# Performance work log

Measured on AMD Instinct MI355X. Metric: run time of the kernel, lower is better.

Reference implementation:

```python
import jax, jax.numpy as jnp
import numpy as np


def _wn(v, g):
    # weight norm over input axis: w[:, j] = g[j] * v[:, j] / ||v[:, j]||
    norm = jnp.sqrt(jnp.sum(v * v, axis=0, keepdims=True))
    return v * (g[None, :] / norm)


def setup_inputs() -> dict:
    key = jax.random.key(0)
    ks = jax.random.split(key, 6)
    M, K1, H, OUT = 65536, 512, 1024, 512
    x = jax.random.normal(ks[0], (M, K1), dtype=jnp.float32)
    v1 = jax.random.normal(ks[1], (K1, H), dtype=jnp.float32) * 0.05
    v2 = jax.random.normal(ks[2], (H, H), dtype=jnp.float32) * 0.05
    v3 = jax.random.normal(ks[3], (H, H), dtype=jnp.float32) * 0.05
    v4 = jax.random.normal(ks[4], (H, H), dtype=jnp.float32) * 0.05
    v5 = jax.random.normal(ks[5], (H, OUT), dtype=jnp.float32) * 0.05
    g1 = jnp.ones((H,), jnp.float32)
    g2 = jnp.ones((H,), jnp.float32)
    g3 = jnp.ones((H,), jnp.float32)
    g4 = jnp.ones((H,), jnp.float32)
    g5 = jnp.ones((OUT,), jnp.float32)
    return {"x": x, "v1": v1, "g1": g1, "v2": v2, "g2": g2,
            "v3": v3, "g3": g3, "v4": v4, "g4": g4, "v5": v5, "g5": g5}


def reference(x, v1, g1, v2, g2, v3, g3, v4, g4, v5, g5):
    w1 = _wn(v1, g1)
    w2 = _wn(v2, g2)
    w3 = _wn(v3, g3)
    w4 = _wn(v4, g4)
    w5 = _wn(v5, g5)
    h1 = jax.nn.softplus(x @ w1)    # [M, H]
    h2 = jax.nn.softplus(h1 @ w2)
    h3 = jax.nn.softplus(h2 @ w3)
    h4 = jax.nn.softplus(h3 @ w4)
    out = h4 @ w5                   # final layer linear
    return out
```

## Files before the change

kernel.cpp:

```cpp
#include <hip/hip_runtime.h>
#include <hip/hip_bf16.h>
#include <cstdint>

typedef unsigned short u16;
typedef __attribute__((ext_vector_type(8))) _Float16 f16x8;
typedef __attribute__((ext_vector_type(4))) float f32x4;
typedef __attribute__((ext_vector_type(8))) unsigned short u16x8;

typedef const __attribute__((address_space(1))) void* gas1p;
typedef __attribute__((address_space(3))) void* las3p;
typedef const __attribute__((address_space(3))) u16* lc16p;

__device__ __forceinline__ void gld_lds16(const void* g, void* l) {
    __builtin_amdgcn_global_load_lds((gas1p)g, (las3p)l, 16, 0, 0);
}

__device__ __forceinline__ f16x8 dsr128(const u16* p) {
    f16x8 r;
    asm volatile("ds_read_b128 %0, %1" : "=v"(r) : "v"((lc16p)p));
    return r;
}

__device__ __forceinline__ u16 f2h(float f) {
    _Float16 h = (_Float16)f;
    return __builtin_bit_cast(u16, h);
}

__global__ void cvt_x_kernel(const float4* __restrict__ x, u16* __restrict__ xb) {
    size_t i = (size_t)blockIdx.x * blockDim.x + threadIdx.x;
    float4 a = x[2 * i];
    float4 b = x[2 * i + 1];
    u16x8 o;
    o[0] = f2h(a.x); o[1] = f2h(a.y); o[2] = f2h(a.z); o[3] = f2h(a.w);
    o[4] = f2h(b.x); o[5] = f2h(b.y); o[6] = f2h(b.z); o[7] = f2h(b.w);
    *(u16x8*)&xb[i * 8] = o;
}

struct WnDesc {
    const float* v; const float* g; u16* wT; float* partial;
    int K; int N; int blk0;
};
struct WnPack { WnDesc d[5]; int nlayer; };

__global__ void wn_partial_all(WnPack p) {
    int b = blockIdx.x;
    int l = 0;
    while (l + 1 < p.nlayer && b >= p.d[l + 1].blk0) l++;
    const WnDesc& d = p.d[l];
    int lb = b - d.blk0;
    int nbx = d.N >> 6;
    int bx = lb % nbx, seg = lb / nbx;

    int lane = threadIdx.x & 63;
    int tr = threadIdx.x >> 6;
    int n = bx * 64 + lane;
    int kseg = d.K >> 3;
    int kbeg = seg * kseg;
    float s = 0.f;
    for (int k = kbeg + tr; k < kbeg + kseg; k += 4) {
        float x = d.v[(size_t)k * d.N + n];
        s += x * x;
    }
    __shared__ float red[4][64];
    red[tr][lane] = s;
    __syncthreads();
    if (tr == 0)
        d.partial[seg * d.N + n] = red[0][lane] + red[1][lane] + red[2][lane] + red[3][lane];
}

__global__ void wn_write_all(WnPack p) {
    int b = blockIdx.x;
    int l = 0;
    while (l + 1 < p.nlayer && b >= p.d[l + 1].blk0) l++;
    const WnDesc& d = p.d[l];
    int lb = b - d.blk0;
    int nbx = d.N >> 6;
    int bx = lb % nbx, seg = lb / nbx;

    int lane = threadIdx.x & 63;
    int tr = threadIdx.x >> 6;
    int n = bx * 64 + lane;
    float s = 0.f;
#pragma unroll
    for (int i = 0; i < 8; i++) s += d.partial[i * d.N + n];
    float sc = d.g[n] / sqrtf(s);

    int kseg = d.K >> 3;
    int kbeg = seg * kseg;
    for (int k = kbeg + tr; k < kbeg + kseg; k += 4)
        d.wT[(size_t)n * d.K + k] = f2h(d.v[(size_t)k * d.N + n] * sc);
}

template<int N, int K, bool ACT, bool OUTF32>
__global__ __launch_bounds__(512, 2) void gemm_mlp(
    const u16* __restrict__ A, const u16* __restrict__ Bt,
    u16* __restrict__ Ch, float* __restrict__ Cf)
{
    constexpr int M = 65536;
    constexpr int NT = K / 64;
    constexpr int NTN = N / 256;
    constexpr int NWG = (M / 256) * NTN;

    __shared__ u16 sA[2][256 * 64];
    __shared__ u16 sB[2][2 * 128 * 64];

    const int bid = blockIdx.x;
    const int wk = (bid & 7) * (NWG >> 3) + (bid >> 3);
    const int tm = wk / NTN, tn = wk % NTN;
    const long m0 = (long)tm * 256;
    const int n0 = tn * 256;

    const int tid = threadIdx.x;
    const int lane = tid & 63;
    const int wid = tid >> 6;
    const int wm = (wid >> 2) * 128;
    const int wn = (wid & 3) * 64;

    const int r8 = tid >> 3;
    const int gcol = ((tid & 7) ^ (r8 & 7)) * 8;
    const u16* Abase = A + (m0 + r8) * (size_t)K + gcol;
    const u16* Bbase = Bt + (size_t)(n0 + ((r8 >> 5) * 64 + (r8 & 31))) * K + gcol;
    const int dst8 = tid * 8;

    auto stA0 = [&](int buf, int t) {
        gld_lds16(Abase + (size_t)t * 64, &sA[buf][0 * 4096 + dst8]);
        gld_lds16(Abase + (size_t)128 * K + (size_t)t * 64, &sA[buf][2 * 4096 + dst8]);
    };
    auto stA1 = [&](int buf, int t) {
        gld_lds16(Abase + (size_t)64 * K + (size_t)t * 64, &sA[buf][1 * 4096 + dst8]);
        gld_lds16(Abase + (size_t)192 * K + (size_t)t * 64, &sA[buf][3 * 4096 + dst8]);
    };
    auto stB0 = [&](int buf, int t) {
        gld_lds16(Bbase + (size_t)t * 64, &sB[buf][dst8]);
        gld_lds16(Bbase + (size_t)128 * K + (size_t)t * 64, &sB[buf][4096 + dst8]);
    };
    auto stB1 = [&](int buf, int t) {
        gld_lds16(Bbase + (size_t)32 * K + (size_t)t * 64, &sB[buf][8192 + dst8]);
        gld_lds16(Bbase + (size_t)160 * K + (size_t)t * 64, &sB[buf][8192 + 4096 + dst8]);
    };

    const int rbase = lane & 15;
    const int co0 = ((lane >> 4) ^ (lane & 7)) * 8;
    const int arow0 = (wm + rbase) * 64 + co0;
    const int brow0 = ((wn >> 6) * 32 + rbase) * 64 + co0;

    f32x4 acc[8][4] = {};
    f16x8 rA0[4][2], rA1[4][2], rB0[2][2], rB1[2][2];

    auto dsrA = [&](f16x8 (&r)[4][2], int buf, int qm) {
#pragma unroll
        for (int i = 0; i < 4; i++) {
            int base = arow0 + (qm * 64 + i * 16) * 64;
            r[i][0] = dsr128(&sA[buf][base]);
            r[i][1] = dsr128(&sA[buf][base ^ 32]);
        }
    };
    auto dsrB = [&](f16x8 (&r)[2][2], int buf, int qn) {
#pragma unroll
        for (int j2 = 0; j2 < 2; j2++) {
            int base = brow0 + qn * 8192 + j2 * 1024;
            r[j2][0] = dsr128(&sB[buf][base]);
            r[j2][1] = dsr128(&sB[buf][base ^ 32]);
        }
    };
    auto mm = [&](f16x8 (&ra)[4][2], f16x8 (&rb)[2][2], int qm, int qn) {
        __builtin_amdgcn_s_setprio(1);
#pragma unroll
        for (int kk = 0; kk < 2; kk++)
#pragma unroll
            for (int i = 0; i < 4; i++)
#pragma unroll
                for (int j2 = 0; j2 < 2; j2++)
                    acc[qm * 4 + i][qn * 2 + j2] = __builtin_amdgcn_mfma_f32_16x16x32_f16(
                        ra[i][kk], rb[j2][kk], acc[qm * 4 + i][qn * 2 + j2], 0, 0, 0);
        __builtin_amdgcn_s_setprio(0);
    };
    auto BAR = [&]() { __builtin_amdgcn_s_barrier(); };
#define LGKM(n) { asm volatile("s_waitcnt lgkmcnt(" #n ")"); __builtin_amdgcn_sched_barrier(0); }
#define VMCNT(n) { asm volatile("s_waitcnt vmcnt(" #n ")"); __builtin_amdgcn_sched_barrier(0); }

    stA0(0, 0); stB0(0, 0); stA1(0, 0); stB1(0, 0);
    stA0(1, 1); stB0(1, 1); stA1(1, 1); stB1(1, 1);
    VMCNT(8);
    BAR();
    dsrA(rA0, 0, 0); dsrB(rB0, 0, 0);
    LGKM(0);
    BAR();

    for (int t = 0; t < NT - 2; t++) {
        const int cur = t & 1, nxt = cur ^ 1;
        dsrB(rB1, cur, 1);
        stA0(cur, t + 2);
        BAR(); LGKM(4);
        mm(rA0, rB0, 0, 0);
        BAR();
        dsrA(rA1, cur, 1);
        stB0(cur, t + 2);
        BAR(); LGKM(8);
        mm(rA0, rB1, 0, 1);
        BAR();
        VMCNT(4);
        dsrA(rA0, nxt, 0);
        BAR(); LGKM(8);
        mm(rA1, rB0, 1, 0);
        BAR();
        dsrB(rB0, nxt, 0);
        stA1(cur, t + 2); stB1(cur, t + 2);
        BAR();
        mm(rA1, rB1, 1, 1);
        LGKM(4);
        BAR();
    }
    {
        const int cur = (NT - 2) & 1, nxt = cur ^ 1;
        dsrB(rB1, cur, 1);
        BAR(); LGKM(4);
        mm(rA0, rB0, 0, 0);
        BAR();
        dsrA(rA1, cur, 1);
        BAR(); LGKM(8);
        mm(rA0, rB1, 0, 1);
        BAR();
        VMCNT(0);
        dsrA(rA0, nxt, 0);
        BAR(); LGKM(8);
        mm(rA1, rB0, 1, 0);
        BAR();
        dsrB(rB0, nxt, 0);
        BAR();
        mm(rA1, rB1, 1, 1);
        LGKM(4);
        BAR();
    }
    {
        const int cur = (NT - 1) & 1;
        dsrB(rB1, cur, 1);
        BAR(); LGKM(4);
        mm(rA0, rB0, 0, 0);
        BAR();
        dsrA(rA1, cur, 1);
        BAR(); LGKM(8);
        mm(rA0, rB1, 0, 1);
        BAR();
        LGKM(0);
        mm(rA1, rB0, 1, 0);
        mm(rA1, rB1, 1, 1);
    }
#undef LGKM
#undef VMCNT

    const long crow0 = m0 + wm + ((lane >> 4) << 2);
    const int ccol0 = n0 + wn + (lane & 15);
#pragma unroll
    for (int fi = 0; fi < 8; fi++) {
#pragma unroll
        for (int r = 0; r < 4; r++) {
            const size_t rowoff = (size_t)(crow0 + fi * 16 + r) * N;
#pragma unroll
            for (int fj = 0; fj < 4; fj++) {
                float v = acc[fi][fj][r];
                if (ACT) v = fmaxf(v, 0.f) + __logf(1.f + __expf(-fabsf(v)));
                if (OUTF32) Cf[rowoff + ccol0 + fj * 16] = v;
                else        Ch[rowoff + ccol0 + fj * 16] = f2h(v);
            }
        }
    }
}

extern "C" void kernel_launch(void* const* d_in, const int* in_sizes, int n_in,
                              void* d_out, int out_size, void* d_ws, size_t ws_size,
                              hipStream_t stream) {
    const float* x  = (const float*)d_in[0];
    const float* v1 = (const float*)d_in[1];
    const float* g1 = (const float*)d_in[2];
    const float* v2 = (const float*)d_in[3];
    const float* g2 = (const float*)d_in[4];
    const float* v3 = (const float*)d_in[5];
    const float* g3 = (const float*)d_in[6];
    const float* v4 = (const float*)d_in[7];
    const float* g4 = (const float*)d_in[8];
    const float* v5 = (const float*)d_in[9];
    const float* g5 = (const float*)d_in[10];
    float* out = (float*)d_out;

    const int M = 65536;
    char* ws = (char*)d_ws;
    u16* bufA = (u16*)(ws);
    u16* bufB = (u16*)(ws + 0x8000000ULL);
    u16* w1T  = (u16*)(ws + 0x10000000ULL);
    u16* w2T  = w1T + 1024 * 512;
    u16* w3T  = w2T + 1024 * 1024;
    u16* w4T  = w3T + 1024 * 1024;
    u16* w5T  = w4T + 1024 * 1024;
    float* part = (float*)(ws + 0x10800000ULL);

    cvt_x_kernel<<<(M * 512) / (256 * 8), 256, 0, stream>>>((const float4*)x, bufB);

    WnPack pk;
    int cum = 0;
    auto mk = [&](int i, const float* v, const float* g, u16* wT, int K, int N) {
        pk.d[i] = WnDesc{v, g, wT, part + i * 8 * 1024, K, N, cum};
        cum += (N / 64) * 8;
    };
    mk(0, v1, g1, w1T, 512, 1024);
    mk(1, v2, g2, w2T, 1024, 1024);
    mk(2, v3, g3, w3T, 1024, 1024);
    mk(3, v4, g4, w4T, 1024, 1024);
    mk(4, v5, g5, w5T, 1024, 512);
    pk.nlayer = 5;

    wn_partial_all<<<cum, 256, 0, stream>>>(pk);
    wn_write_all<<<cum, 256, 0, stream>>>(pk);

    gemm_mlp<1024, 512,  true,  false><<<1024, 512, 0, stream>>>(bufB, w1T, bufA, nullptr);
    gemm_mlp<1024, 1024, true,  false><<<1024, 512, 0, stream>>>(bufA, w2T, bufB, nullptr);
    gemm_mlp<1024, 1024, true,  false><<<1024, 512, 0, stream>>>(bufB, w3T, bufA, nullptr);
    gemm_mlp<1024, 1024, true,  false><<<1024, 512, 0, stream>>>(bufA, w4T, bufB, nullptr);
    gemm_mlp<512,  1024, false, true ><<<512,  512, 0, stream>>>(bufB, w5T, nullptr, out);

    (void)in_sizes; (void)n_in; (void)out_size; (void)ws_size;
}
```

Measured before the change: 704.2 us.

## Make GEMMs walk all N tiles per row block with a continuous K pipeline

Each GEMM now launches 256 workgroups, one per 256-row block. Each workgroup loops over every 256-column N tile, and the double-buffered load/compute pipeline runs continuously across tile boundaries, with an in-loop epilogue that stores results and clears the accumulators. The goal is to remove pipeline prologue and drain costs at each tile and to keep the A row block hot in cache. The trade-off is that on a 256-CU part only one workgroup runs per CU, where the old launch had 1024 blocks at 2 per CU. The epilogue stores now also sit inside the pipeline, where they can stall the next tile's prefetch.

```diff
diff --git a/kernel.cpp b/kernel.cpp
--- a/kernel.cpp
+++ b/kernel.cpp
@@ -92,23 +92,23 @@
 }
 
 template<int N, int K, bool ACT, bool OUTF32>
-__global__ __launch_bounds__(512, 2) void gemm_mlp(
+__global__ __launch_bounds__(512, 2) void gemm_persist(
     const u16* __restrict__ A, const u16* __restrict__ Bt,
     u16* __restrict__ Ch, float* __restrict__ Cf)
 {
     constexpr int M = 65536;
-    constexpr int NT = K / 64;
+    constexpr int NTK = K / 64;
+    constexpr int LOGK = (NTK == 8) ? 3 : 4;
     constexpr int NTN = N / 256;
-    constexpr int NWG = (M / 256) * NTN;
+    constexpr int G = NTK * NTN;
+    constexpr int NWG = M / 256;
 
     __shared__ u16 sA[2][256 * 64];
     __shared__ u16 sB[2][2 * 128 * 64];
 
     const int bid = blockIdx.x;
     const int wk = (bid & 7) * (NWG >> 3) + (bid >> 3);
-    const int tm = wk / NTN, tn = wk % NTN;
-    const long m0 = (long)tm * 256;
-    const int n0 = tn * 256;
+    const long m0 = (long)wk * 256;
 
     const int tid = threadIdx.x;
     const int lane = tid & 63;
@@ -119,24 +119,28 @@
     const int r8 = tid >> 3;
     const int gcol = ((tid & 7) ^ (r8 & 7)) * 8;
     const u16* Abase = A + (m0 + r8) * (size_t)K + gcol;
-    const u16* Bbase = Bt + (size_t)(n0 + ((r8 >> 5) * 64 + (r8 & 31))) * K + gcol;
+    const u16* Bbase = Bt + (size_t)((r8 >> 5) * 64 + (r8 & 31)) * K + gcol;
     const int dst8 = tid * 8;
 
-    auto stA0 = [&](int buf, int t) {
-        gld_lds16(Abase + (size_t)t * 64, &sA[buf][0 * 4096 + dst8]);
-        gld_lds16(Abase + (size_t)128 * K + (size_t)t * 64, &sA[buf][2 * 4096 + dst8]);
-    };
-    auto stA1 = [&](int buf, int t) {
-        gld_lds16(Abase + (size_t)64 * K + (size_t)t * 64, &sA[buf][1 * 4096 + dst8]);
-        gld_lds16(Abase + (size_t)192 * K + (size_t)t * 64, &sA[buf][3 * 4096 + dst8]);
-    };
-    auto stB0 = [&](int buf, int t) {
-        gld_lds16(Bbase + (size_t)t * 64, &sB[buf][dst8]);
-        gld_lds16(Bbase + (size_t)128 * K + (size_t)t * 64, &sB[buf][4096 + dst8]);
-    };
-    auto stB1 = [&](int buf, int t) {
-        gld_lds16(Bbase + (size_t)32 * K + (size_t)t * 64, &sB[buf][8192 + dst8]);
-        gld_lds16(Bbase + (size_t)160 * K + (size_t)t * 64, &sB[buf][8192 + 4096 + dst8]);
+    auto aoff = [&](int gs) { return (size_t)(gs & (NTK - 1)) * 64; };
+    auto boff = [&](int gs) {
+        return (size_t)(gs >> LOGK) * ((size_t)256 * K) + (size_t)(gs & (NTK - 1)) * 64;
+    };
+    auto stA0 = [&](int buf, int gs) {
+        gld_lds16(Abase + aoff(gs), &sA[buf][dst8]);
+        gld_lds16(Abase + (size_t)128 * K + aoff(gs), &sA[buf][2 * 4096 + dst8]);
+    };
+    auto stA1 = [&](int buf, int gs) {
+        gld_lds16(Abase + (size_t)64 * K + aoff(gs), &sA[buf][1 * 4096 + dst8]);
+        gld_lds16(Abase + (size_t)192 * K + aoff(gs), &sA[buf][3 * 4096 + dst8]);
+    };
+    auto stB0 = [&](int buf, int gs) {
+        gld_lds16(Bbase + boff(gs), &sB[buf][dst8]);
+        gld_lds16(Bbase + (size_t)128 * K + boff(gs), &sB[buf][4096 + dst8]);
+    };
+    auto stB1 = [&](int buf, int gs) {
+        gld_lds16(Bbase + (size_t)32 * K + boff(gs), &sB[buf][8192 + dst8]);
+        gld_lds16(Bbase + (size_t)160 * K + boff(gs), &sB[buf][8192 + 4096 + dst8]);
     };
 
     const int rbase = lane & 15;
@@ -177,94 +181,81 @@
     };
     auto BAR = [&]() { __builtin_amdgcn_s_barrier(); };
 #define LGKM(n) { asm volatile("s_waitcnt lgkmcnt(" #n ")"); __builtin_amdgcn_sched_barrier(0); }
-#define VMCNT(n) { asm volatile("s_waitcnt vmcnt(" #n ")"); __builtin_amdgcn_sched_barrier(0); }
+#define VMC(n)  { asm volatile("s_waitcnt vmcnt(" #n ")");  __builtin_amdgcn_sched_barrier(0); }
+
+    auto epilogue = [&](int tn) {
+        const long crow0 = m0 + wm + ((lane >> 4) << 2);
+        const int ccol0 = tn * 256 + wn + (lane & 15);
+#pragma unroll
+        for (int fi = 0; fi < 8; fi++) {
+#pragma unroll
+            for (int r = 0; r < 4; r++) {
+                const size_t rowoff = (size_t)(crow0 + fi * 16 + r) * N;
+#pragma unroll
+                for (int fj = 0; fj < 4; fj++) {
+                    float v = acc[fi][fj][r];
+                    if (ACT) v = fmaxf(v, 0.f) + __logf(1.f + __expf(-fabsf(v)));
+                    if (OUTF32) Cf[rowoff + ccol0 + fj * 16] = v;
+                    else        Ch[rowoff + ccol0 + fj * 16] = f2h(v);
+                }
+            }
+        }
+#pragma unroll
+        for (int i = 0; i < 8; i++)
+#pragma unroll
+            for (int j = 0; j < 4; j++)
+                acc[i][j] = (f32x4){0.f, 0.f, 0.f, 0.f};
+    };
 
     stA0(0, 0); stB0(0, 0); stA1(0, 0); stB1(0, 0);
     stA0(1, 1); stB0(1, 1); stA1(1, 1); stB1(1, 1);
-    VMCNT(8);
+    VMC(4);
     BAR();
     dsrA(rA0, 0, 0); dsrB(rB0, 0, 0);
     LGKM(0);
     BAR();
 
-    for (int t = 0; t < NT - 2; t++) {
-        const int cur = t & 1, nxt = cur ^ 1;
+    for (int g = 0; g < G - 1; g++) {
+        const int cur = g & 1, nxt = cur ^ 1;
+        const bool st = (g < G - 2);
         dsrB(rB1, cur, 1);
-        stA0(cur, t + 2);
+        if (st) stA0(cur, g + 2);
         BAR(); LGKM(4);
         mm(rA0, rB0, 0, 0);
         BAR();
         dsrA(rA1, cur, 1);
-        stB0(cur, t + 2);
+        if (st) stB0(cur, g + 2);
         BAR(); LGKM(8);
         mm(rA0, rB1, 0, 1);
-        BAR();
-        VMCNT(4);
+        if (st) { VMC(4); } else { VMC(2); }
+        BAR();
         dsrA(rA0, nxt, 0);
         BAR(); LGKM(8);
         mm(rA1, rB0, 1, 0);
         BAR();
         dsrB(rB0, nxt, 0);
-        stA1(cur, t + 2); stB1(cur, t + 2);
+        if (st) { stA1(cur, g + 2); stB1(cur, g + 2); }
         BAR();
         mm(rA1, rB1, 1, 1);
-        LGKM(4);
-        BAR();
+        if (st) { VMC(4); } else { VMC(0); }
+        BAR();
+        if ((g & (NTK - 1)) == NTK - 1) epilogue(g >> LOGK);
     }
     {
-        const int cur = (NT - 2) & 1, nxt = cur ^ 1;
+        const int cur = (G - 1) & 1;
         dsrB(rB1, cur, 1);
-        BAR(); LGKM(4);
+        LGKM(4);
         mm(rA0, rB0, 0, 0);
-        BAR();
         dsrA(rA1, cur, 1);
-        BAR(); LGKM(8);
+        LGKM(8);
         mm(rA0, rB1, 0, 1);
-        BAR();
-        VMCNT(0);
-        dsrA(rA0, nxt, 0);
-        BAR(); LGKM(8);
-        mm(rA1, rB0, 1, 0);
-        BAR();
-        dsrB(rB0, nxt, 0);
-        BAR();
-        mm(rA1, rB1, 1, 1);
-        LGKM(4);
-        BAR();
-    }
-    {
-        const int cur = (NT - 1) & 1;
-        dsrB(rB1, cur, 1);
-        BAR(); LGKM(4);
-        mm(rA0, rB0, 0, 0);
-        BAR();
-        dsrA(rA1, cur, 1);
-        BAR(); LGKM(8);
-        mm(rA0, rB1, 0, 1);
-        BAR();
         LGKM(0);
         mm(rA1, rB0, 1, 0);
         mm(rA1, rB1, 1, 1);
+        epilogue(NTN - 1);
     }
 #undef LGKM
-#undef VMCNT
-
-    const long crow0 = m0 + wm + ((lane >> 4) << 2);
-    const int ccol0 = n0 + wn + (lane & 15);
-#pragma unroll
-    for (int fi = 0; fi < 8; fi++) {
-#pragma unroll
-        for (int r = 0; r < 4; r++) {
-            const size_t rowoff = (size_t)(crow0 + fi * 16 + r) * N;
-#pragma unroll
-            for (int fj = 0; fj < 4; fj++) {
-                float v = acc[fi][fj][r];
-                if (ACT) v = fmaxf(v, 0.f) + __logf(1.f + __expf(-fabsf(v)));
-                if (OUTF32) Cf[rowoff + ccol0 + fj * 16] = v;
-                else        Ch[rowoff + ccol0 + fj * 16] = f2h(v);
-            }
-        }
-    }
+#undef VMC
 }
 
 extern "C" void kernel_launch(void* const* d_in, const int* in_sizes, int n_in,
@@ -312,11 +303,11 @@
     wn_partial_all<<<cum, 256, 0, stream>>>(pk);
     wn_write_all<<<cum, 256, 0, stream>>>(pk);
 
-    gemm_mlp<1024, 512,  true,  false><<<1024, 512, 0, stream>>>(bufB, w1T, bufA, nullptr);
-    gemm_mlp<1024, 1024, true,  false><<<1024, 512, 0, stream>>>(bufA, w2T, bufB, nullptr);
-    gemm_mlp<1024, 1024, true,  false><<<1024, 512, 0, stream>>>(bufB, w3T, bufA, nullptr);
-    gemm_mlp<1024, 1024, true,  false><<<1024, 512, 0, stream>>>(bufA, w4T, bufB, nullptr);
-    gemm_mlp<512,  1024, false, true ><<<512,  512, 0, stream>>>(bufB, w5T, nullptr, out);
+    gemm_persist<1024, 512,  true,  false><<<256, 512, 0, stream>>>(bufB, w1T, bufA, nullptr);
+    gemm_persist<1024, 1024, true,  false><<<256, 512, 0, stream>>>(bufA, w2T, bufB, nullptr);
+    gemm_persist<1024, 1024, true,  false><<<256, 512, 0, stream>>>(bufB, w3T, bufA, nullptr);
+    gemm_persist<1024, 1024, true,  false><<<256, 512, 0, stream>>>(bufA, w4T, bufB, nullptr);
+    gemm_persist<512,  1024, false, true ><<<256, 512, 0, stream>>>(bufB, w5T, nullptr, out);
 
     (void)in_sizes; (void)n_in; (void)out_size; (void)ws_size;
 }
```

Measured after the change: 750.8 us. 1.07x slower.

## Load B fragments directly from global into registers, drop B LDS staging

Applied to the files above, without the earlier changes.

The GEMM no longer stages weight tiles in shared memory. Each wave now loads its B fragments straight from global memory into registers, while A stays double-buffered in LDS and is read with immediate-offset ds_read instructions. The pipeline becomes a simpler loop with one barrier per K step. This cuts LDS traffic and footprint, but each wave now issues redundant uncoalesced 16-byte global loads for B and has fewer in-flight stages to hide global latency.

```diff
diff --git a/kernel.cpp b/kernel.cpp
--- a/kernel.cpp
+++ b/kernel.cpp
@@ -15,9 +15,10 @@
     __builtin_amdgcn_global_load_lds((gas1p)g, (las3p)l, 16, 0, 0);
 }
 
-__device__ __forceinline__ f16x8 dsr128(const u16* p) {
+template<int OFF>
+__device__ __forceinline__ f16x8 dsr128o(const u16* p) {
     f16x8 r;
-    asm volatile("ds_read_b128 %0, %1" : "=v"(r) : "v"((lc16p)p));
+    asm volatile("ds_read_b128 %0, %1 offset:%2" : "=v"(r) : "v"((lc16p)p), "i"(OFF));
     return r;
 }
 
@@ -92,7 +93,7 @@
 }
 
 template<int N, int K, bool ACT, bool OUTF32>
-__global__ __launch_bounds__(512, 2) void gemm_mlp(
+__global__ __launch_bounds__(512, 2) void gemm_bl2(
     const u16* __restrict__ A, const u16* __restrict__ Bt,
     u16* __restrict__ Ch, float* __restrict__ Cf)
 {
@@ -102,7 +103,6 @@
     constexpr int NWG = (M / 256) * NTN;
 
     __shared__ u16 sA[2][256 * 64];
-    __shared__ u16 sB[2][2 * 128 * 64];
 
     const int bid = blockIdx.x;
     const int wk = (bid & 7) * (NWG >> 3) + (bid >> 3);
@@ -119,51 +119,33 @@
     const int r8 = tid >> 3;
     const int gcol = ((tid & 7) ^ (r8 & 7)) * 8;
     const u16* Abase = A + (m0 + r8) * (size_t)K + gcol;
-    const u16* Bbase = Bt + (size_t)(n0 + ((r8 >> 5) * 64 + (r8 & 31))) * K + gcol;
     const int dst8 = tid * 8;
-
-    auto stA0 = [&](int buf, int t) {
-        gld_lds16(Abase + (size_t)t * 64, &sA[buf][0 * 4096 + dst8]);
+    auto stA = [&](int buf, int t) {
+        gld_lds16(Abase + (size_t)t * 64, &sA[buf][dst8]);
         gld_lds16(Abase + (size_t)128 * K + (size_t)t * 64, &sA[buf][2 * 4096 + dst8]);
-    };
-    auto stA1 = [&](int buf, int t) {
         gld_lds16(Abase + (size_t)64 * K + (size_t)t * 64, &sA[buf][1 * 4096 + dst8]);
         gld_lds16(Abase + (size_t)192 * K + (size_t)t * 64, &sA[buf][3 * 4096 + dst8]);
-    };
-    auto stB0 = [&](int buf, int t) {
-        gld_lds16(Bbase + (size_t)t * 64, &sB[buf][dst8]);
-        gld_lds16(Bbase + (size_t)128 * K + (size_t)t * 64, &sB[buf][4096 + dst8]);
-    };
-    auto stB1 = [&](int buf, int t) {
-        gld_lds16(Bbase + (size_t)32 * K + (size_t)t * 64, &sB[buf][8192 + dst8]);
-        gld_lds16(Bbase + (size_t)160 * K + (size_t)t * 64, &sB[buf][8192 + 4096 + dst8]);
     };
 
     const int rbase = lane & 15;
     const int co0 = ((lane >> 4) ^ (lane & 7)) * 8;
     const int arow0 = (wm + rbase) * 64 + co0;
-    const int brow0 = ((wn >> 6) * 32 + rbase) * 64 + co0;
+
+    const int bn = n0 + wn + (lane & 15);
+    const int bk = (lane >> 4) * 8;
+    auto ldBg = [&](f16x8 (&dst)[2][2], int qn, int t) {
+#pragma unroll
+        for (int j2 = 0; j2 < 2; j2++)
+#pragma unroll
+            for (int kk = 0; kk < 2; kk++)
+                dst[j2][kk] = *(const f16x8*)&Bt[
+                    (size_t)(bn + qn * 32 + j2 * 16) * K + t * 64 + kk * 32 + bk];
+    };
 
     f32x4 acc[8][4] = {};
-    f16x8 rA0[4][2], rA1[4][2], rB0[2][2], rB1[2][2];
-
-    auto dsrA = [&](f16x8 (&r)[4][2], int buf, int qm) {
-#pragma unroll
-        for (int i = 0; i < 4; i++) {
-            int base = arow0 + (qm * 64 + i * 16) * 64;
-            r[i][0] = dsr128(&sA[buf][base]);
-            r[i][1] = dsr128(&sA[buf][base ^ 32]);
-        }
-    };
-    auto dsrB = [&](f16x8 (&r)[2][2], int buf, int qn) {
-#pragma unroll
-        for (int j2 = 0; j2 < 2; j2++) {
-            int base = brow0 + qn * 8192 + j2 * 1024;
-            r[j2][0] = dsr128(&sB[buf][base]);
-            r[j2][1] = dsr128(&sB[buf][base ^ 32]);
-        }
-    };
-    auto mm = [&](f16x8 (&ra)[4][2], f16x8 (&rb)[2][2], int qm, int qn) {
+    f16x8 rA0[4][2], rA1[4][2], B0[2][2], B1[2][2];
+
+    auto mmq = [&](f16x8 (&ra)[4][2], f16x8 (&rb)[2][2], int qm, int qn) {
         __builtin_amdgcn_s_setprio(1);
 #pragma unroll
         for (int kk = 0; kk < 2; kk++)
@@ -177,77 +159,51 @@
     };
     auto BAR = [&]() { __builtin_amdgcn_s_barrier(); };
 #define LGKM(n) { asm volatile("s_waitcnt lgkmcnt(" #n ")"); __builtin_amdgcn_sched_barrier(0); }
-#define VMCNT(n) { asm volatile("s_waitcnt vmcnt(" #n ")"); __builtin_amdgcn_sched_barrier(0); }
-
-    stA0(0, 0); stB0(0, 0); stA1(0, 0); stB1(0, 0);
-    stA0(1, 1); stB0(1, 1); stA1(1, 1); stB1(1, 1);
-    VMCNT(8);
+#define VMC(n)  { asm volatile("s_waitcnt vmcnt(" #n ")");  __builtin_amdgcn_sched_barrier(0); }
+
+    stA(0, 0);
+    ldBg(B0, 0, 0);
+    ldBg(B1, 1, 0);
+    VMC(8);
     BAR();
-    dsrA(rA0, 0, 0); dsrB(rB0, 0, 0);
-    LGKM(0);
-    BAR();
-
-    for (int t = 0; t < NT - 2; t++) {
+
+    for (int t = 0; t < NT; t++) {
         const int cur = t & 1, nxt = cur ^ 1;
-        dsrB(rB1, cur, 1);
-        stA0(cur, t + 2);
-        BAR(); LGKM(4);
-        mm(rA0, rB0, 0, 0);
-        BAR();
-        dsrA(rA1, cur, 1);
-        stB0(cur, t + 2);
-        BAR(); LGKM(8);
-        mm(rA0, rB1, 0, 1);
-        BAR();
-        VMCNT(4);
-        dsrA(rA0, nxt, 0);
-        BAR(); LGKM(8);
-        mm(rA1, rB0, 1, 0);
-        BAR();
-        dsrB(rB0, nxt, 0);
-        stA1(cur, t + 2); stB1(cur, t + 2);
-        BAR();
-        mm(rA1, rB1, 1, 1);
-        LGKM(4);
-        BAR();
-    }
-    {
-        const int cur = (NT - 2) & 1, nxt = cur ^ 1;
-        dsrB(rB1, cur, 1);
-        BAR(); LGKM(4);
-        mm(rA0, rB0, 0, 0);
-        BAR();
-        dsrA(rA1, cur, 1);
-        BAR(); LGKM(8);
-        mm(rA0, rB1, 0, 1);
-        BAR();
-        VMCNT(0);
-        dsrA(rA0, nxt, 0);
-        BAR(); LGKM(8);
-        mm(rA1, rB0, 1, 0);
-        BAR();
-        dsrB(rB0, nxt, 0);
-        BAR();
-        mm(rA1, rB1, 1, 1);
-        LGKM(4);
-        BAR();
-    }
-    {
-        const int cur = (NT - 1) & 1;
-        dsrB(rB1, cur, 1);
-        BAR(); LGKM(4);
-        mm(rA0, rB0, 0, 0);
-        BAR();
-        dsrA(rA1, cur, 1);
-        BAR(); LGKM(8);
-        mm(rA0, rB1, 0, 1);
-        BAR();
+        const bool more = (t + 1 < NT);
+
+        const u16* pA0 = &sA[cur][arow0];
+        const u16* pA1 = &sA[cur][arow0 ^ 32];
+#pragma unroll
+        for (int i = 0; i < 4; i++) {
+            if (i == 0) { rA0[0][0] = dsr128o<0>(pA0);     rA0[0][1] = dsr128o<0>(pA1); }
+            if (i == 1) { rA0[1][0] = dsr128o<2048>(pA0);  rA0[1][1] = dsr128o<2048>(pA1); }
+            if (i == 2) { rA0[2][0] = dsr128o<4096>(pA0);  rA0[2][1] = dsr128o<4096>(pA1); }
+            if (i == 3) { rA0[3][0] = dsr128o<6144>(pA0);  rA0[3][1] = dsr128o<6144>(pA1); }
+        }
+#pragma unroll
+        for (int i = 0; i < 4; i++) {
+            if (i == 0) { rA1[0][0] = dsr128o<8192>(pA0);  rA1[0][1] = dsr128o<8192>(pA1); }
+            if (i == 1) { rA1[1][0] = dsr128o<10240>(pA0); rA1[1][1] = dsr128o<10240>(pA1); }
+            if (i == 2) { rA1[2][0] = dsr128o<12288>(pA0); rA1[2][1] = dsr128o<12288>(pA1); }
+            if (i == 3) { rA1[3][0] = dsr128o<14336>(pA0); rA1[3][1] = dsr128o<14336>(pA1); }
+        }
+        if (more) stA(nxt, t + 1);
+
+        LGKM(8);
+        mmq(rA0, B0, 0, 0);
+        mmq(rA0, B1, 0, 1);
         LGKM(0);
-        mm(rA1, rB0, 1, 0);
-        mm(rA1, rB1, 1, 1);
+        mmq(rA1, B0, 1, 0);
+        if (more) ldBg(B0, 0, t + 1);
+        mmq(rA1, B1, 1, 1);
+        if (more) {
+            ldBg(B1, 1, t + 1);
+            VMC(8);
+            BAR();
+        }
     }
 #undef LGKM
-#undef VMCNT
+#undef VMC
 
     const long crow0 = m0 + wm + ((lane >> 4) << 2);
     const int ccol0 = n0 + wn + (lane & 15);
@@ -312,11 +268,11 @@
     wn_partial_all<<<cum, 256, 0, stream>>>(pk);
     wn_write_all<<<cum, 256, 0, stream>>>(pk);
 
-    gemm_mlp<1024, 512,  true,  false><<<1024, 512, 0, stream>>>(bufB, w1T, bufA, nullptr);
-    gemm_mlp<1024, 1024, true,  false><<<1024, 512, 0, stream>>>(bufA, w2T, bufB, nullptr);
-    gemm_mlp<1024, 1024, true,  false><<<1024, 512, 0, stream>>>(bufB, w3T, bufA, nullptr);
-    gemm_mlp<1024, 1024, true,  false><<<1024, 512, 0, stream>>>(bufA, w4T, bufB, nullptr);
-    gemm_mlp<512,  1024, false, true ><<<512,  512, 0, stream>>>(bufB, w5T, nullptr, out);
+    gemm_bl2<1024, 512,  true,  false><<<1024, 512, 0, stream>>>(bufB, w1T, bufA, nullptr);
+    gemm_bl2<1024, 1024, true,  false><<<1024, 512, 0, stream>>>(bufA, w2T, bufB, nullptr);
+    gemm_bl2<1024, 1024, true,  false><<<1024, 512, 0, stream>>>(bufB, w3T, bufA, nullptr);
+    gemm_bl2<1024, 1024, true,  false><<<1024, 512, 0, stream>>>(bufA, w4T, bufB, nullptr);
+    gemm_bl2<512,  1024, false, true ><<<512,  512, 0, stream>>>(bufB, w5T, nullptr, out);
 
     (void)in_sizes; (void)n_in; (void)out_size; (void)ws_size;
 }
```

New measurement: 873.8 us. 24.1% more time.
